# Kernel tuning notes

Hardware: AMD Instinct MI355X
Metric: run time of the kernel (lower is better)

Reference implementation:

```python
import jax, jax.numpy as jnp
from jax import lax
import numpy as np

B, N, K = 8, 4096, 64          # clouds, points per cloud, max neighbors
N1, N2 = N // 2, N // 8        # fps ratio 0.5, then 0.25
R1, R2 = 0.2, 0.4              # ball-query radii


def setup_inputs() -> dict:
    key = jax.random.key(0)
    ks = jax.random.split(key, 7)
    def w(k, i, o):
        return jax.random.normal(k, (i, o), jnp.float32) / np.sqrt(i).astype(np.float32)
    return {
        "pos": jax.random.uniform(ks[0], (B, N, 3), jnp.float32),
        "w1a": w(ks[1], 3, 64),    "b1a": jnp.zeros(64, jnp.float32),
        "w1b": w(ks[2], 64, 64),   "b1b": jnp.zeros(64, jnp.float32),
        "w2a": w(ks[3], 67, 128),  "b2a": jnp.zeros(128, jnp.float32),
        "w2b": w(ks[4], 128, 128), "b2b": jnp.zeros(128, jnp.float32),
        "w3a": w(ks[5], 131, 256), "b3a": jnp.zeros(256, jnp.float32),
        "w3b": w(ks[6], 256, 1024),"b3b": jnp.zeros(1024, jnp.float32),
    }


def fps(pos, n_samples):
    # farthest point sampling, deterministic start at index 0. pos: [n, 3]
    d0 = jnp.sum((pos - pos[0]) ** 2, axis=-1)
    def step(mind, _):
        nxt = jnp.argmax(mind)
        d = jnp.sum((pos - pos[nxt]) ** 2, axis=-1)
        return jnp.minimum(mind, d), nxt
    _, idxs = lax.scan(step, d0, None, length=n_samples - 1)
    return jnp.concatenate([jnp.zeros((1,), idxs.dtype), idxs])


def ball_query(centers, pts, r):
    # up to K neighbors within radius r (nearest-first); centers are a subset of pts
    d2 = jnp.sum((centers[:, None, :] - pts[None, :, :]) ** 2, axis=-1)  # [M, n]
    neg = jnp.where(d2 <= r * r, -d2, -jnp.inf)
    vals, nbr = lax.top_k(neg, K)
    return nbr, vals > -jnp.inf  # [M, K] indices, validity mask


def mlp(x, w1, b1, w2, b2, relu_last):
    h = jax.nn.relu(x @ w1 + b1) @ w2 + b2
    return jax.nn.relu(h) if relu_last else h


def masked_max(h, mask):
    # max over neighbor axis; every center has itself as a valid neighbor
    return jnp.max(jnp.where(mask[..., None], h, -jnp.inf), axis=1)


def reference(pos, w1a, b1a, w1b, b1b, w2a, b2a, w2b, b2b, w3a, b3a, w3b, b3b):
    def single(p):  # p: [N, 3]
        # SA1: x is None -> per-edge input is relative position only
        idx1 = fps(p, N1)
        c1 = p[idx1]                                   # [N1, 3]
        nbr1, m1 = ball_query(c1, p, R1)               # [N1, K]
        rel1 = p[nbr1] - c1[:, None, :]                # [N1, K, 3]
        x1 = masked_max(mlp(rel1, w1a, b1a, w1b, b1b, True), m1)   # [N1, 64]
        # SA2: per-edge input is [x_j, pos_j - pos_i]
        idx2 = fps(c1, N2)
        c2 = c1[idx2]                                  # [N2, 3]
        nbr2, m2 = ball_query(c2, c1, R2)              # [N2, K]
        feat2 = jnp.concatenate([x1[nbr2], c1[nbr2] - c2[:, None, :]], axis=-1)  # [N2,K,67]
        x2 = masked_max(mlp(feat2, w2a, b2a, w2b, b2b, True), m2)  # [N2, 128]
        # Global SA: MLP on [x, pos] then global max pool
        g = mlp(jnp.concatenate([x2, c2], axis=-1), w3a, b3a, w3b, b3b, False)   # [N2,1024]
        return jnp.max(g, axis=0)                      # [1024]
    return jax.vmap(single)(pos)                       # [B, 1024]
```

## Files before the change

kernel.cpp:

```cpp
#include <hip/hip_runtime.h>
#include <cstdint>
#include <cstddef>


static constexpr int Bc = 8;
static constexpr int Np = 4096;
static constexpr int Kn = 64;
static constexpr int M1 = 2048;
static constexpr int M2 = 512;
static constexpr int LDX = 132;

#define DEVINL __device__ __forceinline__

DEVINL float d2_exact(float ax, float ay, float az, float bx, float by, float bz) {
    float dx = __fsub_rn(ax, bx);
    float dy = __fsub_rn(ay, by);
    float dz = __fsub_rn(az, bz);
    float xx = __fmul_rn(dx, dx);
    float yy = __fmul_rn(dy, dy);
    float zz = __fmul_rn(dz, dz);
    return __fadd_rn(__fadd_rn(xx, yy), zz);
}

template <int CTRL, int RM, int BM>
DEVINL unsigned long long dpp_max_step(unsigned long long k) {
    unsigned lo = (unsigned)k, hi = (unsigned)(k >> 32);
    unsigned slo = (unsigned)__builtin_amdgcn_update_dpp(0, (int)lo, CTRL, RM, BM, true);
    unsigned shi = (unsigned)__builtin_amdgcn_update_dpp(0, (int)hi, CTRL, RM, BM, true);
    unsigned long long s = ((unsigned long long)shi << 32) | (unsigned long long)slo;
    return s > k ? s : k;
}

DEVINL unsigned long long wave_max_u64_dpp(unsigned long long k) {
    k = dpp_max_step<0x111, 0xf, 0xf>(k);
    k = dpp_max_step<0x112, 0xf, 0xf>(k);
    k = dpp_max_step<0x114, 0xf, 0xf>(k);
    k = dpp_max_step<0x118, 0xf, 0xf>(k);
    k = dpp_max_step<0x142, 0xa, 0xf>(k);
    k = dpp_max_step<0x143, 0xc, 0xf>(k);
    return k;
}

DEVINL unsigned mort3(unsigned v) {
    return (v & 1u) | ((v & 2u) << 2) | ((v & 4u) << 4);
}

DEVINL unsigned cell_of(float x, float y, float z) {
    int ix = (int)(x * 8.0f); ix = ix < 0 ? 0 : (ix > 7 ? 7 : ix);
    int iy = (int)(y * 8.0f); iy = iy < 0 ? 0 : (iy > 7 ? 7 : iy);
    int iz = (int)(z * 8.0f); iz = iz < 0 ? 0 : (iz > 7 ? 7 : iz);
    return mort3((unsigned)ix) | (mort3((unsigned)iy) << 1) | (mort3((unsigned)iz) << 2);
}

DEVINL unsigned* scan512(unsigned* h0, unsigned* h1, int t) {
    unsigned* src = h0; unsigned* dst = h1;
    for (int d = 1; d < 512; d <<= 1) {
        unsigned v = src[t];
        if (t >= d) v += src[t - d];
        dst[t] = v;
        __syncthreads();
        unsigned* tmp = src; src = dst; dst = tmp;
    }
    return src;
}

__global__ __launch_bounds__(512)
void fps2x_kernel(const float* __restrict__ pos, float* __restrict__ c1,
                  float* __restrict__ c2, float* __restrict__ X) {
    constexpr int NT = 512;
    __shared__ float scx[Np], scy[Np], scz[Np];
    __shared__ unsigned spk[Np];
    __shared__ float s2c[M1 * 3];
    __shared__ unsigned h0[512], h1[512];
    __shared__ unsigned long long slots[3];
    const int b = blockIdx.x;
    const int t = threadIdx.x;
    const int lane = t & 63;

    {
        constexpr int PT = Np / NT;
        const float* base = pos + (size_t)b * Np * 3;
        float gx[PT], gy[PT], gz[PT];
        unsigned gc[PT];
        #pragma unroll
        for (int j = 0; j < PT; ++j) {
            int p = j * NT + t;
            gx[j] = base[p * 3 + 0];
            gy[j] = base[p * 3 + 1];
            gz[j] = base[p * 3 + 2];
            gc[j] = cell_of(gx[j], gy[j], gz[j]);
        }
        float x0 = base[0], y0 = base[1], z0 = base[2];
        h0[t] = 0;
        if (t == 0) { slots[0] = 0; slots[1] = 0; slots[2] = 0; }
        __syncthreads();
        #pragma unroll
        for (int j = 0; j < PT; ++j) atomicAdd(&h0[gc[j]], 1u);
        __syncthreads();
        unsigned cnt = h0[t];
        unsigned* inc = scan512(h0, h1, t);
        inc[t] -= cnt;
        __syncthreads();
        #pragma unroll
        for (int j = 0; j < PT; ++j) {
            unsigned p = atomicAdd(&inc[gc[j]], 1u);
            scx[p] = gx[j]; scy[p] = gy[j]; scz[p] = gz[j];
            spk[p] = ((0xFFFu - (unsigned)(j * NT + t)) << 12) | p;
        }
        __syncthreads();

        float px[PT], py[PT], pz[PT], mind[PT];
        unsigned oi[PT];
        #pragma unroll
        for (int j = 0; j < PT; ++j) {
            int p = t * PT + j;
            px[j] = scx[p]; py[j] = scy[p]; pz[j] = scz[p];
            oi[j] = spk[p];
        }
        float lox = px[0], hix = px[0], loy = py[0], hiy = py[0], loz = pz[0], hiz = pz[0];
        #pragma unroll
        for (int j = 1; j < PT; ++j) {
            lox = fminf(lox, px[j]); hix = fmaxf(hix, px[j]);
            loy = fminf(loy, py[j]); hiy = fmaxf(hiy, py[j]);
            loz = fminf(loz, pz[j]); hiz = fmaxf(hiz, pz[j]);
        }

        unsigned long long ck = 0;
        #pragma unroll
        for (int j = 0; j < PT; ++j) {
            float d = d2_exact(px[j], py[j], pz[j], x0, y0, z0);
            mind[j] = d;
            unsigned long long kj =
                ((unsigned long long)__float_as_uint(d) << 24) | (unsigned long long)oi[j];
            if (kj > ck) ck = kj;
        }
        float bmax = __uint_as_float((unsigned)(ck >> 24));
        unsigned long long wkey = wave_max_u64_dpp(ck);
        if (lane == 63) atomicMax(&slots[1], wkey);
        if (t == 0) {
            s2c[0] = x0; s2c[1] = y0; s2c[2] = z0;
        }
        int rd = 1, wr = 2, rs = 0;
        for (int s = 1; s < M1; ++s) {
            __syncthreads();
            unsigned long long km = slots[rd];
            if (t == 0) slots[rs] = 0;
            unsigned spos = (unsigned)km & 0xFFFu;
            float cx = scx[spos], cy = scy[spos], cz = scz[spos];
            if (t == 0) {
                s2c[s * 3 + 0] = cx; s2c[s * 3 + 1] = cy; s2c[s * 3 + 2] = cz;
            }
            float dxv = fmaxf(fmaxf(lox - cx, cx - hix), 0.0f);
            float dyv = fmaxf(fmaxf(loy - cy, cy - hiy), 0.0f);
            float dzv = fmaxf(fmaxf(loz - cz, cz - hiz), 0.0f);
            float L = dxv * dxv + dyv * dyv + dzv * dzv;
            bool fire = (L * 0.999f <= bmax);
            if (fire) {
                unsigned long long nck = 0;
                #pragma unroll
                for (int j = 0; j < PT; ++j) {
                    float d = d2_exact(px[j], py[j], pz[j], cx, cy, cz);
                    float m = fminf(mind[j], d);
                    mind[j] = m;
                    unsigned long long kj =
                        ((unsigned long long)__float_as_uint(m) << 24) | (unsigned long long)oi[j];
                    if (kj > nck) nck = kj;
                }
                ck = nck;
                bmax = __uint_as_float((unsigned)(ck >> 24));
            }
            if (__ballot(fire) != 0ull) wkey = wave_max_u64_dpp(ck);
            if (lane == 63) atomicMax(&slots[wr], wkey);
            int nrd = wr; wr = rs; rs = rd; rd = nrd;
        }
    }
    __syncthreads();

    for (int i = t; i < M1 * 3; i += 512)
        c1[(size_t)b * M1 * 3 + i] = s2c[i];

    {
        constexpr int PT = M1 / NT;
        float* c2buf = s2c;
        float gx[PT], gy[PT], gz[PT];
        unsigned gc[PT];
        #pragma unroll
        for (int j = 0; j < PT; ++j) {
            int p = j * NT + t;
            gx[j] = s2c[p * 3 + 0];
            gy[j] = s2c[p * 3 + 1];
            gz[j] = s2c[p * 3 + 2];
            gc[j] = cell_of(gx[j], gy[j], gz[j]);
        }
        float x0 = s2c[0], y0 = s2c[1], z0 = s2c[2];
        h0[t] = 0;
        if (t == 0) { slots[0] = 0; slots[1] = 0; slots[2] = 0; }
        __syncthreads();
        #pragma unroll
        for (int j = 0; j < PT; ++j) atomicAdd(&h0[gc[j]], 1u);
        __syncthreads();
        unsigned cnt = h0[t];
        unsigned* inc = scan512(h0, h1, t);
        inc[t] -= cnt;
        __syncthreads();
        #pragma unroll
        for (int j = 0; j < PT; ++j) {
            unsigned p = atomicAdd(&inc[gc[j]], 1u);
            scx[p] = gx[j]; scy[p] = gy[j]; scz[p] = gz[j];
            spk[p] = ((0xFFFu - (unsigned)(j * NT + t)) << 12) | p;
        }
        __syncthreads();

        float px[PT], py[PT], pz[PT], mind[PT];
        unsigned oi[PT];
        #pragma unroll
        for (int j = 0; j < PT; ++j) {
            int p = t * PT + j;
            px[j] = scx[p]; py[j] = scy[p]; pz[j] = scz[p];
            oi[j] = spk[p];
        }
        float lox = px[0], hix = px[0], loy = py[0], hiy = py[0], loz = pz[0], hiz = pz[0];
        #pragma unroll
        for (int j = 1; j < PT; ++j) {
            lox = fminf(lox, px[j]); hix = fmaxf(hix, px[j]);
            loy = fminf(loy, py[j]); hiy = fmaxf(hiy, py[j]);
            loz = fminf(loz, pz[j]); hiz = fmaxf(hiz, pz[j]);
        }

        unsigned long long ck = 0;
        #pragma unroll
        for (int j = 0; j < PT; ++j) {
            float d = d2_exact(px[j], py[j], pz[j], x0, y0, z0);
            mind[j] = d;
            unsigned long long kj =
                ((unsigned long long)__float_as_uint(d) << 24) | (unsigned long long)oi[j];
            if (kj > ck) ck = kj;
        }
        float bmax = __uint_as_float((unsigned)(ck >> 24));
        unsigned long long wkey = wave_max_u64_dpp(ck);
        if (lane == 63) atomicMax(&slots[1], wkey);
        if (t == 0) {
            c2buf[0] = x0; c2buf[1] = y0; c2buf[2] = z0;
        }
        int rd = 1, wr = 2, rs = 0;
        for (int s = 1; s < M2; ++s) {
            __syncthreads();
            unsigned long long km = slots[rd];
            if (t == 0) slots[rs] = 0;
            unsigned spos = (unsigned)km & 0xFFFu;
            float cx = scx[spos], cy = scy[spos], cz = scz[spos];
            if (t == 0) {
                c2buf[s * 3 + 0] = cx; c2buf[s * 3 + 1] = cy; c2buf[s * 3 + 2] = cz;
            }
            float dxv = fmaxf(fmaxf(lox - cx, cx - hix), 0.0f);
            float dyv = fmaxf(fmaxf(loy - cy, cy - hiy), 0.0f);
            float dzv = fmaxf(fmaxf(loz - cz, cz - hiz), 0.0f);
            float L = dxv * dxv + dyv * dyv + dzv * dzv;
            bool fire = (L * 0.999f <= bmax);
            if (fire) {
                unsigned long long nck = 0;
                #pragma unroll
                for (int j = 0; j < PT; ++j) {
                    float d = d2_exact(px[j], py[j], pz[j], cx, cy, cz);
                    float m = fminf(mind[j], d);
                    mind[j] = m;
                    unsigned long long kj =
                        ((unsigned long long)__float_as_uint(m) << 24) | (unsigned long long)oi[j];
                    if (kj > nck) nck = kj;
                }
                ck = nck;
                bmax = __uint_as_float((unsigned)(ck >> 24));
            }
            if (__ballot(fire) != 0ull) wkey = wave_max_u64_dpp(ck);
            if (lane == 63) atomicMax(&slots[wr], wkey);
            int nrd = wr; wr = rs; rs = rd; rd = nrd;
        }
        __syncthreads();

        for (int i = t; i < M2 * 3; i += 512)
            c2[(size_t)b * M2 * 3 + i] = c2buf[i];
        for (int i = t; i < M2 * 3; i += 512) {
            int s = i / 3, k = i - s * 3;
            X[(size_t)(b * M2 + s) * LDX + 128 + k] = c2buf[i];
        }
    }
}

template <int NPT>
__global__ __launch_bounds__(256)
void bq_kernel(const float* __restrict__ pts, const float* __restrict__ ctr,
               int mshift, float r2, int* __restrict__ nbr) {
    constexpr int CH = NPT / 64;
    constexpr int CAP = 1024;
    __shared__ uint2 cbuf[4][CAP];
    const int lane = threadIdx.x & 63;
    const int wl = threadIdx.x >> 6;
    int w = __builtin_amdgcn_readfirstlane((int)(blockIdx.x * 4 + wl));
    const int b = w >> mshift;
    const float* pb = pts + (size_t)b * NPT * 3;
    const float* cp = ctr + (size_t)w * 3;
    float cx = cp[0], cy = cp[1], cz = cp[2];
    const unsigned r2b = __float_as_uint(r2);

    unsigned ub[CH];
    int cnt = 0;
    #pragma unroll
    for (int j = 0; j < CH; ++j) {
        int p = j * 64 + lane;
        float d = d2_exact(pb[p * 3 + 0], pb[p * 3 + 1], pb[p * 3 + 2], cx, cy, cz);
        ub[j] = __float_as_uint(d);
        cnt += __popcll(__ballot(ub[j] <= r2b));
    }
    int* out = nbr + (size_t)w * Kn;
    const unsigned long long lml = (1ull << lane) - 1ull;

    if (cnt <= Kn) {
        int basep = 0;
        #pragma unroll
        for (int j = 0; j < CH; ++j) {
            bool v = ub[j] <= r2b;
            unsigned long long mk = __ballot(v);
            if (v) out[basep + __popcll(mk & lml)] = j * 64 + lane;
            basep += __popcll(mk);
        }
        if (lane >= cnt) out[lane] = -1;
    } else if (cnt <= CAP) {
        uint2* buf = cbuf[wl];
        int basep = 0;
        #pragma unroll
        for (int j = 0; j < CH; ++j) {
            bool v = ub[j] <= r2b;
            unsigned long long mk = __ballot(v);
            if (v) buf[basep + __popcll(mk & lml)] =
                       make_uint2(ub[j], (unsigned)(j * 64 + lane));
            basep += __popcll(mk);
        }
        const int C2 = (cnt + 63) >> 6;
        unsigned cb[CAP / 64], ci[CAP / 64];
        #pragma unroll
        for (int e = 0; e < CAP / 64; ++e) {
            if (e >= C2) break;
            int p = e * 64 + lane;
            uint2 v = buf[p];
            cb[e] = (p < cnt) ? v.x : 0xFFFFFFFFu;
            ci[e] = v.y;
        }
        unsigned lo = 0, hi = r2b;
        while (lo < hi) {
            unsigned mid = lo + ((hi - lo) >> 1);
            int c = 0;
            #pragma unroll
            for (int e = 0; e < CAP / 64; ++e) {
                if (e >= C2) break;
                c += __popcll(__ballot(cb[e] <= mid));
            }
            if (c >= Kn) hi = mid; else lo = mid + 1;
        }
        const unsigned tt = lo;
        int cntLess = 0;
        #pragma unroll
        for (int e = 0; e < CAP / 64; ++e) {
            if (e >= C2) break;
            cntLess += __popcll(__ballot(cb[e] < tt));
        }
        const int quota = Kn - cntLess;
        int baseLt = 0, eqseen = 0;
        #pragma unroll
        for (int e = 0; e < CAP / 64; ++e) {
            if (e >= C2) break;
            bool lt = cb[e] < tt;
            bool eq = cb[e] == tt;
            unsigned long long mlt = __ballot(lt);
            unsigned long long meq = __ballot(eq);
            if (lt) out[baseLt + __popcll(mlt & lml)] = (int)ci[e];
            if (eq) {
                int rr = eqseen + __popcll(meq & lml);
                if (rr < quota) out[cntLess + rr] = (int)ci[e];
            }
            baseLt += __popcll(mlt);
            eqseen += __popcll(meq);
        }
    } else {
        unsigned lo = 0, hi = r2b;
        while (lo < hi) {
            unsigned mid = lo + ((hi - lo) >> 1);
            int c = 0;
            #pragma unroll
            for (int j = 0; j < CH; ++j) c += __popcll(__ballot(ub[j] <= mid));
            if (c >= Kn) hi = mid; else lo = mid + 1;
        }
        const unsigned tt = lo;
        int cntLess = 0;
        #pragma unroll
        for (int j = 0; j < CH; ++j) cntLess += __popcll(__ballot(ub[j] < tt));
        const int quota = Kn - cntLess;
        int baseLt = 0, eqseen = 0;
        #pragma unroll
        for (int j = 0; j < CH; ++j) {
            bool lt = ub[j] < tt;
            bool eq = ub[j] == tt;
            unsigned long long mlt = __ballot(lt);
            unsigned long long meq = __ballot(eq);
            if (lt) out[baseLt + __popcll(mlt & lml)] = j * 64 + lane;
            if (eq) {
                int rr = eqseen + __popcll(meq & lml);
                if (rr < quota) out[cntLess + rr] = j * 64 + lane;
            }
            baseLt += __popcll(mlt);
            eqseen += __popcll(meq);
        }
    }
}

__global__ __launch_bounds__(256)
void mlp1_kernel(const float* __restrict__ pos, const float* __restrict__ c1,
                 const int* __restrict__ nbr, const float* __restrict__ w1aT,
                 const float* __restrict__ w1bT, const float* __restrict__ b1b,
                 float* __restrict__ x1) {
    const int lane = threadIdx.x & 63;
    int w = __builtin_amdgcn_readfirstlane((int)(blockIdx.x * 4 + (threadIdx.x >> 6)));
    const int b = w >> 11;
    const int ii = nbr[(size_t)w * Kn + lane];
    const bool valid = ii >= 0;
    const int i2 = valid ? ii : 0;
    const float* pp = pos + ((size_t)b * Np + i2) * 3;
    const float* cc = c1 + (size_t)w * 3;
    float rx = pp[0] - cc[0], ry = pp[1] - cc[1], rz = pp[2] - cc[2];
    float h1[64];
    #pragma unroll
    for (int h = 0; h < 64; ++h) {
        float4 wv = ((const float4*)w1aT)[h];
        float a = fmaf(rx, wv.x, fmaf(ry, wv.y, fmaf(rz, wv.z, wv.w)));
        h1[h] = fmaxf(a, 0.0f);
    }
    float* orow = x1 + (size_t)w * 64;
    for (int c4 = 0; c4 < 16; ++c4) {
        float v4[4];
        #pragma unroll
        for (int cq = 0; cq < 4; ++cq) {
            int c = c4 * 4 + cq;
            float acc = b1b[c];
            const float4* wr = (const float4*)(w1bT + (size_t)c * 64);
            #pragma unroll
            for (int q = 0; q < 16; ++q) {
                float4 wv = wr[q];
                acc = fmaf(h1[4 * q + 0], wv.x, acc);
                acc = fmaf(h1[4 * q + 1], wv.y, acc);
                acc = fmaf(h1[4 * q + 2], wv.z, acc);
                acc = fmaf(h1[4 * q + 3], wv.w, acc);
            }
            float v = fmaxf(acc, 0.0f);
            v = valid ? v : -__builtin_inff();
            #pragma unroll
            for (int o = 32; o > 0; o >>= 1) v = fmaxf(v, __shfl_xor(v, o, 64));
            v4[cq] = v;
        }
        if (lane == 0)
            ((float4*)orow)[c4] = make_float4(v4[0], v4[1], v4[2], v4[3]);
    }
}

__global__ __launch_bounds__(256)
void mlp2_kernel(const float* __restrict__ x1, const float* __restrict__ c1,
                 const float* __restrict__ c2, const int* __restrict__ nbr2,
                 const float* __restrict__ w2aT, const float* __restrict__ w2bT,
                 const float* __restrict__ b2b, float* __restrict__ X) {
    const int lane = threadIdx.x & 63;
    int w = __builtin_amdgcn_readfirstlane((int)(blockIdx.x * 4 + (threadIdx.x >> 6)));
    const int b = w >> 9;
    const int ii = nbr2[(size_t)w * Kn + lane];
    const bool valid = ii >= 0;
    const int i2 = valid ? ii : 0;

    float x[68];
    const float4* xr = (const float4*)(x1 + ((size_t)b * M1 + i2) * 64);
// ... 85 lines not shown
    const int col0 = nt * 64;
    const int t = threadIdx.x;
    const int rg = t >> 5, cg = t & 31;

    float acc[4][2] = {{0.f, 0.f}, {0.f, 0.f}, {0.f, 0.f}, {0.f, 0.f}};
    for (int k0 = 0; k0 < 256; k0 += 32) {
        #pragma unroll
        for (int q = 0; q < 4; ++q) {
            int id = t + q * 256;
            As[id >> 5][id & 31] = H[(size_t)(row0 + (id >> 5)) * 256 + k0 + (id & 31)];
        }
        #pragma unroll
        for (int q = 0; q < 8; ++q) {
            int id = t + q * 256;
            Bs[id >> 6][id & 63] = w3b[(size_t)(k0 + (id >> 6)) * 1024 + col0 + (id & 63)];
        }
        __syncthreads();
        #pragma unroll
        for (int kk = 0; kk < 32; ++kk) {
            float b0 = Bs[kk][cg * 2 + 0];
            float b1 = Bs[kk][cg * 2 + 1];
            #pragma unroll
            for (int j = 0; j < 4; ++j) {
                float a = As[rg * 4 + j][kk];
                acc[j][0] = fmaf(a, b0, acc[j][0]);
                acc[j][1] = fmaf(a, b1, acc[j][1]);
            }
        }
        __syncthreads();
    }
    float m0 = fmaxf(fmaxf(acc[0][0], acc[1][0]), fmaxf(acc[2][0], acc[3][0]));
    float m1 = fmaxf(fmaxf(acc[0][1], acc[1][1]), fmaxf(acc[2][1], acc[3][1]));
    red[rg][cg * 2 + 0] = m0;
    red[rg][cg * 2 + 1] = m1;
    __syncthreads();
    if (t < 64) {
        float v = red[0][t];
        #pragma unroll
        for (int q = 1; q < 8; ++q) v = fmaxf(v, red[q][t]);
        part[((size_t)b * 16 + mt) * 1024 + col0 + t] = v;
    }
}

__global__ __launch_bounds__(256)
void rmax_kernel(const float* __restrict__ part, const float* __restrict__ b3b,
                 float* __restrict__ out) {
    int i = blockIdx.x * 256 + threadIdx.x;
    int b = i >> 10, c = i & 1023;
    float v = -__builtin_inff();
    #pragma unroll
    for (int tt = 0; tt < 16; ++tt)
        v = fmaxf(v, part[((size_t)b * 16 + tt) * 1024 + c]);
    out[i] = v + b3b[c];
}

__global__ __launch_bounds__(256)
void prep_kernel(const float* __restrict__ w1a, const float* __restrict__ b1a,
                 const float* __restrict__ w1b, const float* __restrict__ w2a,
                 const float* __restrict__ b2a, const float* __restrict__ w2b,
                 float* __restrict__ w1aT, float* __restrict__ w1bT,
                 float* __restrict__ w2aT, float* __restrict__ w2bT) {
    int i = blockIdx.x * 256 + threadIdx.x;
    if (i < 64 * 4) {
        int h = i >> 2, d = i & 3;
        w1aT[i] = (d < 3) ? w1a[d * 64 + h] : b1a[h];
    }
    if (i < 64 * 64) {
        int c = i >> 6, h = i & 63;
        w1bT[i] = w1b[h * 64 + c];
    }
    if (i < 128 * 80) {
        int h = i / 80, d = i - h * 80;
        w2aT[i] = (d < 67) ? w2a[d * 128 + h] : ((d == 67) ? b2a[h] : 0.0f);
    }
    {
        int c = i >> 7, h = i & 127;
        w2bT[i] = w2b[h * 128 + c];
    }
}

extern "C" void kernel_launch(void* const* d_in, const int* in_sizes, int n_in,
                              void* d_out, int out_size, void* d_ws, size_t ws_size,
                              hipStream_t stream) {
    const float* pos = (const float*)d_in[0];
    const float* w1a = (const float*)d_in[1];
    const float* b1a = (const float*)d_in[2];
    const float* w1b = (const float*)d_in[3];
    const float* b1b = (const float*)d_in[4];
    const float* w2a = (const float*)d_in[5];
    const float* b2a = (const float*)d_in[6];
    const float* w2b = (const float*)d_in[7];
    const float* b2b = (const float*)d_in[8];
    const float* w3a = (const float*)d_in[9];
    const float* b3a = (const float*)d_in[10];
    const float* w3b = (const float*)d_in[11];
    const float* b3b = (const float*)d_in[12];
    float* out = (float*)d_out;

    char* ws = (char*)d_ws;
    size_t off = 0;
    auto alloc = [&](size_t bytes) -> char* {
        char* p = ws + off;
        off += (bytes + 255) & ~(size_t)255;
        return p;
    };
    float* c1   = (float*)alloc(sizeof(float) * Bc * M1 * 3);
    float* c2   = (float*)alloc(sizeof(float) * Bc * M2 * 3);
    int*   nbr1 = (int*)alloc(sizeof(int) * Bc * M1 * Kn);
    int*   nbr2 = (int*)alloc(sizeof(int) * Bc * M2 * Kn);
    float* x1   = (float*)alloc(sizeof(float) * Bc * M1 * 64);
    float* X    = (float*)alloc(sizeof(float) * Bc * M2 * LDX);
    float* H    = (float*)alloc(sizeof(float) * Bc * M2 * 256);
    float* part = (float*)alloc(sizeof(float) * Bc * 16 * 1024);
    float* w1aT = (float*)alloc(sizeof(float) * 64 * 4);
    float* w1bT = (float*)alloc(sizeof(float) * 64 * 64);
    float* w2aT = (float*)alloc(sizeof(float) * 128 * 80);
    float* w2bT = (float*)alloc(sizeof(float) * 128 * 128);

    prep_kernel<<<dim3(64), dim3(256), 0, stream>>>(w1a, b1a, w1b, w2a, b2a, w2b,
                                                    w1aT, w1bT, w2aT, w2bT);
    fps2x_kernel<<<dim3(Bc), dim3(512), 0, stream>>>(pos, c1, c2, X);
    bq_kernel<Np><<<dim3(Bc * M1 / 4), dim3(256), 0, stream>>>(
        pos, c1, 11, (float)(0.2 * 0.2), nbr1);
    mlp1_kernel<<<dim3(Bc * M1 / 4), dim3(256), 0, stream>>>(
        pos, c1, nbr1, w1aT, w1bT, b1b, x1);
    bq_kernel<M1><<<dim3(Bc * M2 / 4), dim3(256), 0, stream>>>(
        c1, c2, 9, (float)(0.4 * 0.4), nbr2);
    mlp2_kernel<<<dim3(Bc * M2 / 4), dim3(256), 0, stream>>>(
        x1, c1, c2, nbr2, w2aT, w2bT, b2b, X);
    gemm1_kernel<<<dim3(Bc * M2), dim3(256), 0, stream>>>(X, w3a, b3a, H);
    gemm2_kernel<<<dim3(Bc * 16 * 16), dim3(256), 0, stream>>>(H, w3b, part);
    rmax_kernel<<<dim3(32), dim3(256), 0, stream>>>(part, b3b, out);
}
```

Before: 2.569 ms.

## Replace FPS shared atomicMax argmax with per-wave slots and 32-bit DPP reduction

In both farthest-point-sampling loops, the 64-bit packed key reduction is split into a 32-bit DPP max on the distance bits plus a tie-break on the index, using readlane and ballot. The shared-memory atomicMax into a triple-buffered slot is replaced by each wave writing its candidate to a double-buffered per-wave array, which every thread then reduces over 8 entries after the barrier. This removes the 64-bit DPP pairs, the LDS atomics and the slot-reset bookkeeping from the serial per-sample critical path. In exchange each thread does extra vector LDS loads and compares per step, and the tie-break path adds a second reduction when distances collide.

After: 2.741 ms. 6.7% more time.

```diff
diff --git a/kernel.cpp b/kernel.cpp
--- a/kernel.cpp
+++ b/kernel.cpp
@@ -23,22 +23,33 @@
 }
 
 template <int CTRL, int RM, int BM>
-DEVINL unsigned long long dpp_max_step(unsigned long long k) {
-    unsigned lo = (unsigned)k, hi = (unsigned)(k >> 32);
-    unsigned slo = (unsigned)__builtin_amdgcn_update_dpp(0, (int)lo, CTRL, RM, BM, true);
-    unsigned shi = (unsigned)__builtin_amdgcn_update_dpp(0, (int)hi, CTRL, RM, BM, true);
-    unsigned long long s = ((unsigned long long)shi << 32) | (unsigned long long)slo;
-    return s > k ? s : k;
-}
-
-DEVINL unsigned long long wave_max_u64_dpp(unsigned long long k) {
-    k = dpp_max_step<0x111, 0xf, 0xf>(k);
-    k = dpp_max_step<0x112, 0xf, 0xf>(k);
-    k = dpp_max_step<0x114, 0xf, 0xf>(k);
-    k = dpp_max_step<0x118, 0xf, 0xf>(k);
-    k = dpp_max_step<0x142, 0xa, 0xf>(k);
-    k = dpp_max_step<0x143, 0xc, 0xf>(k);
-    return k;
+DEVINL unsigned dpp_max_u32_step(unsigned v) {
+    unsigned s = (unsigned)__builtin_amdgcn_update_dpp(0, (int)v, CTRL, RM, BM, true);
+    return s > v ? s : v;
+}
+
+DEVINL unsigned wave_max_u32_dpp(unsigned v) {
+    v = dpp_max_u32_step<0x111, 0xf, 0xf>(v);
+    v = dpp_max_u32_step<0x112, 0xf, 0xf>(v);
+    v = dpp_max_u32_step<0x114, 0xf, 0xf>(v);
+    v = dpp_max_u32_step<0x118, 0xf, 0xf>(v);
+    v = dpp_max_u32_step<0x142, 0xa, 0xf>(v);
+    v = dpp_max_u32_step<0x143, 0xc, 0xf>(v);
+    return v;
+}
+
+DEVINL void wave_reduce_cand(unsigned ch, unsigned cl, unsigned& wh, unsigned& wl) {
+    unsigned h = wave_max_u32_dpp(ch);
+    wh = (unsigned)__builtin_amdgcn_readlane((int)h, 63);
+    unsigned long long mask = __ballot(ch == wh);
+    if (__popcll(mask) == 1) {
+        int ln = __ffsll((unsigned long long)mask) - 1;
+        wl = (unsigned)__builtin_amdgcn_readlane((int)cl, ln);
+    } else {
+        unsigned lm = (ch == wh) ? cl : 0u;
+        lm = wave_max_u32_dpp(lm);
+        wl = (unsigned)__builtin_amdgcn_readlane((int)lm, 63);
+    }
 }
 
 DEVINL unsigned mort3(unsigned v) {
@@ -72,10 +83,11 @@
     __shared__ unsigned spk[Np];
     __shared__ float s2c[M1 * 3];
     __shared__ unsigned h0[512], h1[512];
-    __shared__ unsigned long long slots[3];
+    __shared__ __align__(16) unsigned long long wslot[2][8];
     const int b = blockIdx.x;
     const int t = threadIdx.x;
     const int lane = t & 63;
+    const int wid = t >> 6;
 
     {
         constexpr int PT = Np / NT;
@@ -92,7 +104,6 @@
         }
         float x0 = base[0], y0 = base[1], z0 = base[2];
         h0[t] = 0;
-        if (t == 0) { slots[0] = 0; slots[1] = 0; slots[2] = 0; }
         __syncthreads();
         #pragma unroll
         for (int j = 0; j < PT; ++j) atomicAdd(&h0[gc[j]], 1u);
@@ -125,27 +136,39 @@
             loz = fminf(loz, pz[j]); hiz = fmaxf(hiz, pz[j]);
         }
 
-        unsigned long long ck = 0;
+        unsigned ch = 0, cl = 0;
         #pragma unroll
         for (int j = 0; j < PT; ++j) {
             float d = d2_exact(px[j], py[j], pz[j], x0, y0, z0);
             mind[j] = d;
-            unsigned long long kj =
-                ((unsigned long long)__float_as_uint(d) << 24) | (unsigned long long)oi[j];
-            if (kj > ck) ck = kj;
-        }
-        float bmax = __uint_as_float((unsigned)(ck >> 24));
-        unsigned long long wkey = wave_max_u64_dpp(ck);
-        if (lane == 63) atomicMax(&slots[1], wkey);
+            unsigned db = __float_as_uint(d);
+            ch = db > ch ? db : ch;
+        }
+        #pragma unroll
+        for (int j = 0; j < PT; ++j)
+            if (__float_as_uint(mind[j]) == ch && oi[j] > cl) cl = oi[j];
+        float bmax = __uint_as_float(ch);
+
+        unsigned cwh, cwl;
+        wave_reduce_cand(ch, cl, cwh, cwl);
+        if (lane == 0)
+            wslot[1][wid] = (((unsigned long long)cwh) << 32) | cwl;
         if (t == 0) {
             s2c[0] = x0; s2c[1] = y0; s2c[2] = z0;
         }
-        int rd = 1, wr = 2, rs = 0;
         for (int s = 1; s < M1; ++s) {
             __syncthreads();
-            unsigned long long km = slots[rd];
-            if (t == 0) slots[rs] = 0;
-            unsigned spos = (unsigned)km & 0xFFFu;
+            int rb = s & 1;
+            const ulonglong2* sp = (const ulonglong2*)&wslot[rb][0];
+            ulonglong2 q0 = sp[0], q1 = sp[1], q2 = sp[2], q3 = sp[3];
+            unsigned long long m0 = q0.x > q0.y ? q0.x : q0.y;
+            unsigned long long m1 = q1.x > q1.y ? q1.x : q1.y;
+            unsigned long long m2 = q2.x > q2.y ? q2.x : q2.y;
+            unsigned long long m3 = q3.x > q3.y ? q3.x : q3.y;
+            m0 = m0 > m1 ? m0 : m1;
+            m2 = m2 > m3 ? m2 : m3;
+            unsigned long long wk = m0 > m2 ? m0 : m2;
+            unsigned spos = (unsigned)wk & 0xFFFu;
             float cx = scx[spos], cy = scy[spos], cz = scz[spos];
             if (t == 0) {
                 s2c[s * 3 + 0] = cx; s2c[s * 3 + 1] = cy; s2c[s * 3 + 2] = cz;
@@ -156,22 +179,25 @@
             float L = dxv * dxv + dyv * dyv + dzv * dzv;
             bool fire = (L * 0.999f <= bmax);
             if (fire) {
-                unsigned long long nck = 0;
+                unsigned nh = 0;
                 #pragma unroll
                 for (int j = 0; j < PT; ++j) {
                     float d = d2_exact(px[j], py[j], pz[j], cx, cy, cz);
                     float m = fminf(mind[j], d);
                     mind[j] = m;
-                    unsigned long long kj =
-                        ((unsigned long long)__float_as_uint(m) << 24) | (unsigned long long)oi[j];
-                    if (kj > nck) nck = kj;
+                    unsigned mb = __float_as_uint(m);
+                    nh = mb > nh ? mb : nh;
                 }
-                ck = nck;
-                bmax = __uint_as_float((unsigned)(ck >> 24));
-            }
-            if (__ballot(fire) != 0ull) wkey = wave_max_u64_dpp(ck);
-            if (lane == 63) atomicMax(&slots[wr], wkey);
-            int nrd = wr; wr = rs; rs = rd; rd = nrd;
+                unsigned nl = 0;
+                #pragma unroll
+                for (int j = 0; j < PT; ++j)
+                    if (__float_as_uint(mind[j]) == nh && oi[j] > nl) nl = oi[j];
+                ch = nh; cl = nl;
+                bmax = __uint_as_float(ch);
+            }
+            if (__ballot(fire) != 0ull) wave_reduce_cand(ch, cl, cwh, cwl);
+            if (lane == 0)
+                wslot[rb ^ 1][wid] = (((unsigned long long)cwh) << 32) | cwl;
         }
     }
     __syncthreads();
@@ -194,7 +220,6 @@
         }
         float x0 = s2c[0], y0 = s2c[1], z0 = s2c[2];
         h0[t] = 0;
-        if (t == 0) { slots[0] = 0; slots[1] = 0; slots[2] = 0; }
         __syncthreads();
         #pragma unroll
         for (int j = 0; j < PT; ++j) atomicAdd(&h0[gc[j]], 1u);
@@ -227,27 +252,39 @@
             loz = fminf(loz, pz[j]); hiz = fmaxf(hiz, pz[j]);
         }
 
-        unsigned long long ck = 0;
+        unsigned ch = 0, cl = 0;
         #pragma unroll
         for (int j = 0; j < PT; ++j) {
             float d = d2_exact(px[j], py[j], pz[j], x0, y0, z0);
             mind[j] = d;
-            unsigned long long kj =
-                ((unsigned long long)__float_as_uint(d) << 24) | (unsigned long long)oi[j];
-            if (kj > ck) ck = kj;
-        }
-        float bmax = __uint_as_float((unsigned)(ck >> 24));
-        unsigned long long wkey = wave_max_u64_dpp(ck);
-        if (lane == 63) atomicMax(&slots[1], wkey);
+            unsigned db = __float_as_uint(d);
+            ch = db > ch ? db : ch;
+        }
+        #pragma unroll
+        for (int j = 0; j < PT; ++j)
+            if (__float_as_uint(mind[j]) == ch && oi[j] > cl) cl = oi[j];
+        float bmax = __uint_as_float(ch);
+
+        unsigned cwh, cwl;
+        wave_reduce_cand(ch, cl, cwh, cwl);
+        if (lane == 0)
+            wslot[1][wid] = (((unsigned long long)cwh) << 32) | cwl;
         if (t == 0) {
             c2buf[0] = x0; c2buf[1] = y0; c2buf[2] = z0;
         }
-        int rd = 1, wr = 2, rs = 0;
         for (int s = 1; s < M2; ++s) {
             __syncthreads();
-            unsigned long long km = slots[rd];
-            if (t == 0) slots[rs] = 0;
-            unsigned spos = (unsigned)km & 0xFFFu;
+            int rb = s & 1;
+            const ulonglong2* sp = (const ulonglong2*)&wslot[rb][0];
+            ulonglong2 q0 = sp[0], q1 = sp[1], q2 = sp[2], q3 = sp[3];
+            unsigned long long m0 = q0.x > q0.y ? q0.x : q0.y;
+            unsigned long long m1 = q1.x > q1.y ? q1.x : q1.y;
+            unsigned long long m2 = q2.x > q2.y ? q2.x : q2.y;
+            unsigned long long m3 = q3.x > q3.y ? q3.x : q3.y;
+            m0 = m0 > m1 ? m0 : m1;
+            m2 = m2 > m3 ? m2 : m3;
+            unsigned long long wk = m0 > m2 ? m0 : m2;
+            unsigned spos = (unsigned)wk & 0xFFFu;
             float cx = scx[spos], cy = scy[spos], cz = scz[spos];
             if (t == 0) {
                 c2buf[s * 3 + 0] = cx; c2buf[s * 3 + 1] = cy; c2buf[s * 3 + 2] = cz;
@@ -258,22 +295,25 @@
             float L = dxv * dxv + dyv * dyv + dzv * dzv;
             bool fire = (L * 0.999f <= bmax);
             if (fire) {
-                unsigned long long nck = 0;
+                unsigned nh = 0;
                 #pragma unroll
                 for (int j = 0; j < PT; ++j) {
                     float d = d2_exact(px[j], py[j], pz[j], cx, cy, cz);
                     float m = fminf(mind[j], d);
                     mind[j] = m;
-                    unsigned long long kj =
-                        ((unsigned long long)__float_as_uint(m) << 24) | (unsigned long long)oi[j];
-                    if (kj > nck) nck = kj;
+                    unsigned mb = __float_as_uint(m);
+                    nh = mb > nh ? mb : nh;
                 }
-                ck = nck;
-                bmax = __uint_as_float((unsigned)(ck >> 24));
-            }
-            if (__ballot(fire) != 0ull) wkey = wave_max_u64_dpp(ck);
-            if (lane == 63) atomicMax(&slots[wr], wkey);
-            int nrd = wr; wr = rs; rs = rd; rd = nrd;
+                unsigned nl = 0;
+                #pragma unroll
+                for (int j = 0; j < PT; ++j)
+                    if (__float_as_uint(mind[j]) == nh && oi[j] > nl) nl = oi[j];
+                ch = nh; cl = nl;
+                bmax = __uint_as_float(ch);
+            }
+            if (__ballot(fire) != 0ull) wave_reduce_cand(ch, cl, cwh, cwl);
+            if (lane == 0)
+                wslot[rb ^ 1][wid] = (((unsigned long long)cwh) << 32) | cwl;
         }
         __syncthreads();
 
```

## Split FPS stages and co-schedule them with independent ball-query and MLP work

Applied to the files above, without the earlier changes.

The two-stage FPS kernel is split. Stage one is merged with the weight-prep kernel as extra blocks. Stage two runs in its own 256-thread block alongside the SA1 ball-query blocks in the same launch, since both depend only on c1. The SA2 ball query is likewise fused with the SA1 MLP, so the long serial FPS2 loop on 8 blocks overlaps with the independent parallel work and the launch count drops. Point storage moves to a packed float4 LDS layout for single-load center fetches. In exchange, the 256-thread FPS2 has more points per thread, and the fused kernels carry the larger LDS of their biggest role.

New measurement: 2.393 ms. -6.8%, faster.

```diff
diff --git a/kernel.cpp b/kernel.cpp
--- a/kernel.cpp
+++ b/kernel.cpp
@@ -64,238 +64,165 @@
     return src;
 }
 
+DEVINL unsigned* scan512x256(unsigned* h0, unsigned* h1, int t) {
+    unsigned* src = h0; unsigned* dst = h1;
+    for (int d = 1; d < 512; d <<= 1) {
+        unsigned a = src[t];
+        unsigned b = src[t + 256];
+        if (t >= d) a += src[t - d];
+        b += src[t + 256 - d];
+        dst[t] = a; dst[t + 256] = b;
+        __syncthreads();
+        unsigned* tmp = src; src = dst; dst = tmp;
+    }
+    return src;
+}
+
 __global__ __launch_bounds__(512)
-void fps2x_kernel(const float* __restrict__ pos, float* __restrict__ c1,
-                  float* __restrict__ c2, float* __restrict__ X) {
-    constexpr int NT = 512;
-    __shared__ float scx[Np], scy[Np], scz[Np];
-    __shared__ unsigned spk[Np];
+void fps1_prep_kernel(const float* __restrict__ pos, float* __restrict__ c1,
+                      const float* __restrict__ w1a, const float* __restrict__ b1a,
+                      const float* __restrict__ w1b, const float* __restrict__ w2a,
+                      const float* __restrict__ b2a, const float* __restrict__ w2b,
+                      float* __restrict__ w1aT, float* __restrict__ w1bT,
+                      float* __restrict__ w2aT, float* __restrict__ w2bT) {
+    __shared__ float4 scp[Np];
     __shared__ float s2c[M1 * 3];
     __shared__ unsigned h0[512], h1[512];
     __shared__ unsigned long long slots[3];
+    const int t = threadIdx.x;
+
+    if (blockIdx.x >= Bc) {
+        int i = (int)(blockIdx.x - Bc) * 512 + t;
+        if (i < 64 * 4) {
+            int h = i >> 2, d = i & 3;
+            w1aT[i] = (d < 3) ? w1a[d * 64 + h] : b1a[h];
+        }
+        if (i < 64 * 64) {
+            int c = i >> 6, h = i & 63;
+            w1bT[i] = w1b[h * 64 + c];
+        }
+        if (i < 128 * 80) {
+            int h = i / 80, d = i - h * 80;
+            w2aT[i] = (d < 67) ? w2a[d * 128 + h] : ((d == 67) ? b2a[h] : 0.0f);
+        }
+        {
+            int c = i >> 7, h = i & 127;
+            w2bT[i] = w2b[h * 128 + c];
+        }
+        return;
+    }
+
     const int b = blockIdx.x;
-    const int t = threadIdx.x;
     const int lane = t & 63;
-
-    {
-        constexpr int PT = Np / NT;
-        const float* base = pos + (size_t)b * Np * 3;
-        float gx[PT], gy[PT], gz[PT];
-        unsigned gc[PT];
-        #pragma unroll
-        for (int j = 0; j < PT; ++j) {
-            int p = j * NT + t;
-            gx[j] = base[p * 3 + 0];
-            gy[j] = base[p * 3 + 1];
-            gz[j] = base[p * 3 + 2];
-            gc[j] = cell_of(gx[j], gy[j], gz[j]);
-        }
-        float x0 = base[0], y0 = base[1], z0 = base[2];
-        h0[t] = 0;
-        if (t == 0) { slots[0] = 0; slots[1] = 0; slots[2] = 0; }
+    constexpr int NT = 512;
+    constexpr int PT = Np / NT;
+
+    const float* base = pos + (size_t)b * Np * 3;
+    float gx[PT], gy[PT], gz[PT];
+    unsigned gc[PT];
+    #pragma unroll
+    for (int j = 0; j < PT; ++j) {
+        int p = j * NT + t;
+        gx[j] = base[p * 3 + 0];
+        gy[j] = base[p * 3 + 1];
+        gz[j] = base[p * 3 + 2];
+        gc[j] = cell_of(gx[j], gy[j], gz[j]);
+    }
+    float x0 = base[0], y0 = base[1], z0 = base[2];
+    h0[t] = 0;
+    if (t == 0) { slots[0] = 0; slots[1] = 0; slots[2] = 0; }
+    __syncthreads();
+    #pragma unroll
+    for (int j = 0; j < PT; ++j) atomicAdd(&h0[gc[j]], 1u);
+    __syncthreads();
+    unsigned cnt = h0[t];
+    unsigned* inc = scan512(h0, h1, t);
+    inc[t] -= cnt;
+    __syncthreads();
+    #pragma unroll
+    for (int j = 0; j < PT; ++j) {
+        unsigned p = atomicAdd(&inc[gc[j]], 1u);
+        unsigned key = ((0xFFFu - (unsigned)(j * NT + t)) << 12) | p;
+        scp[p] = make_float4(gx[j], gy[j], gz[j], __uint_as_float(key));
+    }
+    __syncthreads();
+
+    float px[PT], py[PT], pz[PT], mind[PT];
+    unsigned oi[PT];
+    #pragma unroll
+    for (int j = 0; j < PT; ++j) {
+        float4 v = scp[t * PT + j];
+        px[j] = v.x; py[j] = v.y; pz[j] = v.z;
+        oi[j] = __float_as_uint(v.w);
+    }
+    float lox = px[0], hix = px[0], loy = py[0], hiy = py[0], loz = pz[0], hiz = pz[0];
+    #pragma unroll
+    for (int j = 1; j < PT; ++j) {
+        lox = fminf(lox, px[j]); hix = fmaxf(hix, px[j]);
+        loy = fminf(loy, py[j]); hiy = fmaxf(hiy, py[j]);
+        loz = fminf(loz, pz[j]); hiz = fmaxf(hiz, pz[j]);
+    }
+
+    unsigned long long ck = 0;
+    #pragma unroll
+    for (int j = 0; j < PT; ++j) {
+        float d = d2_exact(px[j], py[j], pz[j], x0, y0, z0);
+        mind[j] = d;
+        unsigned long long kj =
+            ((unsigned long long)__float_as_uint(d) << 24) | (unsigned long long)oi[j];
+        if (kj > ck) ck = kj;
+    }
+    float bmax = __uint_as_float((unsigned)(ck >> 24));
+    unsigned long long wkey = wave_max_u64_dpp(ck);
+    if (lane == 63) atomicMax(&slots[1], wkey);
+    if (t == 0) {
+        s2c[0] = x0; s2c[1] = y0; s2c[2] = z0;
+    }
+    int rd = 1, wr = 2, rs = 0;
+    for (int s = 1; s < M1; ++s) {
         __syncthreads();
-        #pragma unroll
-        for (int j = 0; j < PT; ++j) atomicAdd(&h0[gc[j]], 1u);
-        __syncthreads();
-        unsigned cnt = h0[t];
-        unsigned* inc = scan512(h0, h1, t);
-        inc[t] -= cnt;
-        __syncthreads();
-        #pragma unroll
-        for (int j = 0; j < PT; ++j) {
-            unsigned p = atomicAdd(&inc[gc[j]], 1u);
-            scx[p] = gx[j]; scy[p] = gy[j]; scz[p] = gz[j];
-            spk[p] = ((0xFFFu - (unsigned)(j * NT + t)) << 12) | p;
-        }
-        __syncthreads();
-
-        float px[PT], py[PT], pz[PT], mind[PT];
-        unsigned oi[PT];
-        #pragma unroll
-        for (int j = 0; j < PT; ++j) {
-            int p = t * PT + j;
-            px[j] = scx[p]; py[j] = scy[p]; pz[j] = scz[p];
-            oi[j] = spk[p];
-        }
-        float lox = px[0], hix = px[0], loy = py[0], hiy = py[0], loz = pz[0], hiz = pz[0];
-        #pragma unroll
-        for (int j = 1; j < PT; ++j) {
-            lox = fminf(lox, px[j]); hix = fmaxf(hix, px[j]);
-            loy = fminf(loy, py[j]); hiy = fmaxf(hiy, py[j]);
-            loz = fminf(loz, pz[j]); hiz = fmaxf(hiz, pz[j]);
-        }
-
-        unsigned long long ck = 0;
-        #pragma unroll
-        for (int j = 0; j < PT; ++j) {
-            float d = d2_exact(px[j], py[j], pz[j], x0, y0, z0);
-            mind[j] = d;
-            unsigned long long kj =
-                ((unsigned long long)__float_as_uint(d) << 24) | (unsigned long long)oi[j];
-            if (kj > ck) ck = kj;
-        }
-        float bmax = __uint_as_float((unsigned)(ck >> 24));
-        unsigned long long wkey = wave_max_u64_dpp(ck);
-        if (lane == 63) atomicMax(&slots[1], wkey);
+        unsigned long long km = slots[rd];
+        if (t == 0) slots[rs] = 0;
+        unsigned spos = (unsigned)km & 0xFFFu;
+        float4 cc = scp[spos];
+        float cx = cc.x, cy = cc.y, cz = cc.z;
         if (t == 0) {
-            s2c[0] = x0; s2c[1] = y0; s2c[2] = z0;
-        }
-        int rd = 1, wr = 2, rs = 0;
-        for (int s = 1; s < M1; ++s) {
-            __syncthreads();
-            unsigned long long km = slots[rd];
-            if (t == 0) slots[rs] = 0;
-            unsigned spos = (unsigned)km & 0xFFFu;
-            float cx = scx[spos], cy = scy[spos], cz = scz[spos];
-            if (t == 0) {
-                s2c[s * 3 + 0] = cx; s2c[s * 3 + 1] = cy; s2c[s * 3 + 2] = cz;
+            s2c[s * 3 + 0] = cx; s2c[s * 3 + 1] = cy; s2c[s * 3 + 2] = cz;
+        }
+        float dxv = fmaxf(fmaxf(lox - cx, cx - hix), 0.0f);
+        float dyv = fmaxf(fmaxf(loy - cy, cy - hiy), 0.0f);
+        float dzv = fmaxf(fmaxf(loz - cz, cz - hiz), 0.0f);
+        float L = dxv * dxv + dyv * dyv + dzv * dzv;
+        bool fire = (L * 0.999f <= bmax);
+        if (fire) {
+            unsigned long long nck = 0;
+            #pragma unroll
+            for (int j = 0; j < PT; ++j) {
+                float d = d2_exact(px[j], py[j], pz[j], cx, cy, cz);
+                float m = fminf(mind[j], d);
+                mind[j] = m;
+                unsigned long long kj =
+                    ((unsigned long long)__float_as_uint(m) << 24) | (unsigned long long)oi[j];
+                if (kj > nck) nck = kj;
             }
-            float dxv = fmaxf(fmaxf(lox - cx, cx - hix), 0.0f);
-            float dyv = fmaxf(fmaxf(loy - cy, cy - hiy), 0.0f);
-            float dzv = fmaxf(fmaxf(loz - cz, cz - hiz), 0.0f);
-            float L = dxv * dxv + dyv * dyv + dzv * dzv;
-            bool fire = (L * 0.999f <= bmax);
-            if (fire) {
-                unsigned long long nck = 0;
-                #pragma unroll
-                for (int j = 0; j < PT; ++j) {
-                    float d = d2_exact(px[j], py[j], pz[j], cx, cy, cz);
-                    float m = fminf(mind[j], d);
-                    mind[j] = m;
-                    unsigned long long kj =
-                        ((unsigned long long)__float_as_uint(m) << 24) | (unsigned long long)oi[j];
-                    if (kj > nck) nck = kj;
-                }
-                ck = nck;
-                bmax = __uint_as_float((unsigned)(ck >> 24));
-            }
-            if (__ballot(fire) != 0ull) wkey = wave_max_u64_dpp(ck);
-            if (lane == 63) atomicMax(&slots[wr], wkey);
-            int nrd = wr; wr = rs; rs = rd; rd = nrd;
-        }
-    }
-    __syncthreads();
-
+            ck = nck;
+            bmax = __uint_as_float((unsigned)(ck >> 24));
+        }
+        if (__ballot(fire) != 0ull) wkey = wave_max_u64_dpp(ck);
+        if (lane == 63) atomicMax(&slots[wr], wkey);
+        int nrd = wr; wr = rs; rs = rd; rd = nrd;
+    }
+    __syncthreads();
     for (int i = t; i < M1 * 3; i += 512)
         c1[(size_t)b * M1 * 3 + i] = s2c[i];
-
-    {
-        constexpr int PT = M1 / NT;
-        float* c2buf = s2c;
-        float gx[PT], gy[PT], gz[PT];
-        unsigned gc[PT];
-        #pragma unroll
-        for (int j = 0; j < PT; ++j) {
-            int p = j * NT + t;
-            gx[j] = s2c[p * 3 + 0];
-            gy[j] = s2c[p * 3 + 1];
-            gz[j] = s2c[p * 3 + 2];
-            gc[j] = cell_of(gx[j], gy[j], gz[j]);
-        }
-        float x0 = s2c[0], y0 = s2c[1], z0 = s2c[2];
-        h0[t] = 0;
-        if (t == 0) { slots[0] = 0; slots[1] = 0; slots[2] = 0; }
-        __syncthreads();
-        #pragma unroll
-        for (int j = 0; j < PT; ++j) atomicAdd(&h0[gc[j]], 1u);
-        __syncthreads();
-        unsigned cnt = h0[t];
-        unsigned* inc = scan512(h0, h1, t);
-        inc[t] -= cnt;
-        __syncthreads();
-        #pragma unroll
-        for (int j = 0; j < PT; ++j) {
-            unsigned p = atomicAdd(&inc[gc[j]], 1u);
-            scx[p] = gx[j]; scy[p] = gy[j]; scz[p] = gz[j];
-            spk[p] = ((0xFFFu - (unsigned)(j * NT + t)) << 12) | p;
-        }
-        __syncthreads();
-
-        float px[PT], py[PT], pz[PT], mind[PT];
-        unsigned oi[PT];
-        #pragma unroll
-        for (int j = 0; j < PT; ++j) {
-            int p = t * PT + j;
-            px[j] = scx[p]; py[j] = scy[p]; pz[j] = scz[p];
-            oi[j] = spk[p];
-        }
-        float lox = px[0], hix = px[0], loy = py[0], hiy = py[0], loz = pz[0], hiz = pz[0];
-        #pragma unroll
-        for (int j = 1; j < PT; ++j) {
-            lox = fminf(lox, px[j]); hix = fmaxf(hix, px[j]);
-            loy = fminf(loy, py[j]); hiy = fmaxf(hiy, py[j]);
-            loz = fminf(loz, pz[j]); hiz = fmaxf(hiz, pz[j]);
-        }
-
-        unsigned long long ck = 0;
-        #pragma unroll
-        for (int j = 0; j < PT; ++j) {
-            float d = d2_exact(px[j], py[j], pz[j], x0, y0, z0);
-            mind[j] = d;
-            unsigned long long kj =
-                ((unsigned long long)__float_as_uint(d) << 24) | (unsigned long long)oi[j];
-            if (kj > ck) ck = kj;
-        }
-        float bmax = __uint_as_float((unsigned)(ck >> 24));
-        unsigned long long wkey = wave_max_u64_dpp(ck);
-        if (lane == 63) atomicMax(&slots[1], wkey);
-        if (t == 0) {
-            c2buf[0] = x0; c2buf[1] = y0; c2buf[2] = z0;
-        }
-        int rd = 1, wr = 2, rs = 0;
-        for (int s = 1; s < M2; ++s) {
-            __syncthreads();
-            unsigned long long km = slots[rd];
-            if (t == 0) slots[rs] = 0;
-            unsigned spos = (unsigned)km & 0xFFFu;
-            float cx = scx[spos], cy = scy[spos], cz = scz[spos];
-            if (t == 0) {
-                c2buf[s * 3 + 0] = cx; c2buf[s * 3 + 1] = cy; c2buf[s * 3 + 2] = cz;
-            }
-            float dxv = fmaxf(fmaxf(lox - cx, cx - hix), 0.0f);
-            float dyv = fmaxf(fmaxf(loy - cy, cy - hiy), 0.0f);
-            float dzv = fmaxf(fmaxf(loz - cz, cz - hiz), 0.0f);
-            float L = dxv * dxv + dyv * dyv + dzv * dzv;
-            bool fire = (L * 0.999f <= bmax);
-            if (fire) {
-                unsigned long long nck = 0;
-                #pragma unroll
-                for (int j = 0; j < PT; ++j) {
-                    float d = d2_exact(px[j], py[j], pz[j], cx, cy, cz);
-                    float m = fminf(mind[j], d);
-                    mind[j] = m;
-                    unsigned long long kj =
-                        ((unsigned long long)__float_as_uint(m) << 24) | (unsigned long long)oi[j];
-                    if (kj > nck) nck = kj;
-                }
-                ck = nck;
-                bmax = __uint_as_float((unsigned)(ck >> 24));
-            }
-            if (__ballot(fire) != 0ull) wkey = wave_max_u64_dpp(ck);
-            if (lane == 63) atomicMax(&slots[wr], wkey);
-            int nrd = wr; wr = rs; rs = rd; rd = nrd;
-        }
-        __syncthreads();
-
-        for (int i = t; i < M2 * 3; i += 512)
-            c2[(size_t)b * M2 * 3 + i] = c2buf[i];
-        for (int i = t; i < M2 * 3; i += 512) {
-            int s = i / 3, k = i - s * 3;
-            X[(size_t)(b * M2 + s) * LDX + 128 + k] = c2buf[i];
-        }
-    }
 }
 
 template <int NPT>
-__global__ __launch_bounds__(256)
-void bq_kernel(const float* __restrict__ pts, const float* __restrict__ ctr,
-               int mshift, float r2, int* __restrict__ nbr) {
+DEVINL void bq_body(const float* __restrict__ pts, const float* __restrict__ ctr,
+                    int mshift, float r2, int* __restrict__ nbr,
+                    uint2* __restrict__ buf, int w, int lane) {
     constexpr int CH = NPT / 64;
     constexpr int CAP = 1024;
-    __shared__ uint2 cbuf[4][CAP];
-    const int lane = threadIdx.x & 63;
-    const int wl = threadIdx.x >> 6;
-    int w = __builtin_amdgcn_readfirstlane((int)(blockIdx.x * 4 + wl));
     const int b = w >> mshift;
     const float* pb = pts + (size_t)b * NPT * 3;
     const float* cp = ctr + (size_t)w * 3;
@@ -325,7 +252,6 @@
         }
         if (lane >= cnt) out[lane] = -1;
     } else if (cnt <= CAP) {
-        uint2* buf = cbuf[wl];
         int basep = 0;
         #pragma unroll
         for (int j = 0; j < CH; ++j) {
@@ -412,15 +338,159 @@
     }
 }
 
+static constexpr int K2_LDS = 43040;
+
 __global__ __launch_bounds__(256)
-void mlp1_kernel(const float* __restrict__ pos, const float* __restrict__ c1,
-                 const int* __restrict__ nbr, const float* __restrict__ w1aT,
-                 const float* __restrict__ w1bT, const float* __restrict__ b1b,
-                 float* __restrict__ x1) {
-    const int lane = threadIdx.x & 63;
-    int w = __builtin_amdgcn_readfirstlane((int)(blockIdx.x * 4 + (threadIdx.x >> 6)));
+void fps2_bq1_kernel(const float* __restrict__ pos, const float* __restrict__ c1,
+                     float* __restrict__ c2, float* __restrict__ X,
+                     int* __restrict__ nbr1) {
+    extern __shared__ char smem[];
+    const int t = threadIdx.x;
+    const int lane = t & 63;
+
+    if (blockIdx.x >= Bc) {
+        uint2* buf = (uint2*)smem + (size_t)(t >> 6) * 1024;
+        int w = __builtin_amdgcn_readfirstlane(
+            (int)(blockIdx.x - Bc) * 4 + (t >> 6));
+        bq_body<Np>(pos, c1, 11, (float)(0.2 * 0.2), nbr1, buf, w, lane);
+        return;
+    }
+
+    float4* scp2 = (float4*)smem;
+    float* c2buf = (float*)(smem + 32768);
+    unsigned* h0 = (unsigned*)(smem + 38912);
+    unsigned* h1 = (unsigned*)(smem + 40960);
+    unsigned long long* slots = (unsigned long long*)(smem + 43008);
+
+    const int b = blockIdx.x;
+    constexpr int NT = 256;
+    constexpr int PT = M1 / NT;
+    const float* base = c1 + (size_t)b * M1 * 3;
+
+    float gx[PT], gy[PT], gz[PT];
+    unsigned gc[PT];
+    #pragma unroll
+    for (int j = 0; j < PT; ++j) {
+        int p = j * NT + t;
+        gx[j] = base[p * 3 + 0];
+        gy[j] = base[p * 3 + 1];
+        gz[j] = base[p * 3 + 2];
+        gc[j] = cell_of(gx[j], gy[j], gz[j]);
+    }
+    float x0 = base[0], y0 = base[1], z0 = base[2];
+    h0[t] = 0; h0[t + 256] = 0;
+    if (t == 0) { slots[0] = 0; slots[1] = 0; slots[2] = 0; }
+    __syncthreads();
+    #pragma unroll
+    for (int j = 0; j < PT; ++j) atomicAdd(&h0[gc[j]], 1u);
+    __syncthreads();
+    unsigned cnt0 = h0[t], cnt1 = h0[t + 256];
+    unsigned* inc = scan512x256(h0, h1, t);
+    inc[t] -= cnt0; inc[t + 256] -= cnt1;
+    __syncthreads();
+    #pragma unroll
+    for (int j = 0; j < PT; ++j) {
+        unsigned p = atomicAdd(&inc[gc[j]], 1u);
+        unsigned key = ((0xFFFu - (unsigned)(j * NT + t)) << 12) | p;
+        scp2[p] = make_float4(gx[j], gy[j], gz[j], __uint_as_float(key));
+    }
+    __syncthreads();
+
+    float px[PT], py[PT], pz[PT], mind[PT];
+    unsigned oi[PT];
+    #pragma unroll
+    for (int j = 0; j < PT; ++j) {
+        float4 v = scp2[t * PT + j];
+        px[j] = v.x; py[j] = v.y; pz[j] = v.z;
+        oi[j] = __float_as_uint(v.w);
+    }
+    float lox = px[0], hix = px[0], loy = py[0], hiy = py[0], loz = pz[0], hiz = pz[0];
+    #pragma unroll
+    for (int j = 1; j < PT; ++j) {
+        lox = fminf(lox, px[j]); hix = fmaxf(hix, px[j]);
+        loy = fminf(loy, py[j]); hiy = fmaxf(hiy, py[j]);
+        loz = fminf(loz, pz[j]); hiz = fmaxf(hiz, pz[j]);
+    }
+
+    unsigned long long ck = 0;
+    #pragma unroll
+    for (int j = 0; j < PT; ++j) {
+        float d = d2_exact(px[j], py[j], pz[j], x0, y0, z0);
+        mind[j] = d;
+        unsigned long long kj =
+            ((unsigned long long)__float_as_uint(d) << 24) | (unsigned long long)oi[j];
+        if (kj > ck) ck = kj;
+    }
+    float bmax = __uint_as_float((unsigned)(ck >> 24));
+    unsigned long long wkey = wave_max_u64_dpp(ck);
+    if (lane == 63) atomicMax(&slots[1], wkey);
+    if (t == 0) {
+        c2buf[0] = x0; c2buf[1] = y0; c2buf[2] = z0;
+    }
+    int rd = 1, wr = 2, rs = 0;
+    for (int s = 1; s < M2; ++s) {
+        __syncthreads();
+        unsigned long long km = slots[rd];
+        if (t == 0) slots[rs] = 0;
+        unsigned spos = (unsigned)km & 0xFFFu;
+        float4 cc = scp2[spos];
+        float cx = cc.x, cy = cc.y, cz = cc.z;
+        if (t == 0) {
+            c2buf[s * 3 + 0] = cx; c2buf[s * 3 + 1] = cy; c2buf[s * 3 + 2] = cz;
+        }
+        float dxv = fmaxf(fmaxf(lox - cx, cx - hix), 0.0f);
+        float dyv = fmaxf(fmaxf(loy - cy, cy - hiy), 0.0f);
+        float dzv = fmaxf(fmaxf(loz - cz, cz - hiz), 0.0f);
+        float L = dxv * dxv + dyv * dyv + dzv * dzv;
+        bool fire = (L * 0.999f <= bmax);
+        if (fire) {
+            unsigned long long nck = 0;
+            #pragma unroll
+            for (int j = 0; j < PT; ++j) {
+                float d = d2_exact(px[j], py[j], pz[j], cx, cy, cz);
+                float m = fminf(mind[j], d);
+                mind[j] = m;
+                unsigned long long kj =
+                    ((unsigned long long)__float_as_uint(m) << 24) | (unsigned long long)oi[j];
+                if (kj > nck) nck = kj;
+            }
+            ck = nck;
+            bmax = __uint_as_float((unsigned)(ck >> 24));
+        }
+        if (__ballot(fire) != 0ull) wkey = wave_max_u64_dpp(ck);
+        if (lane == 63) atomicMax(&slots[wr], wkey);
+        int nrd = wr; wr = rs; rs = rd; rd = nrd;
+    }
+    __syncthreads();
+    for (int i = t; i < M2 * 3; i += 256)
+        c2[(size_t)b * M2 * 3 + i] = c2buf[i];
+    for (int i = t; i < M2 * 3; i += 256) {
+        int s = i / 3, k = i - s * 3;
+        X[(size_t)(b * M2 + s) * LDX + 128 + k] = c2buf[i];
+    }
+}
+
+__global__ __launch_bounds__(256)
+void bq2_mlp1_kernel(const float* __restrict__ pos, const float* __restrict__ c1,
+                     const float* __restrict__ c2, int* __restrict__ nbr2,
+                     const int* __restrict__ nbr1, const float* __restrict__ w1aT,
+                     const float* __restrict__ w1bT, const float* __restrict__ b1b,
+                     float* __restrict__ x1) {
+    __shared__ uint2 cbuf[4][1024];
+    const int t = threadIdx.x;
+    const int lane = t & 63;
+    constexpr int NBQ2 = Bc * M2 / 4;
+
+    if (blockIdx.x < NBQ2) {
+        int w = __builtin_amdgcn_readfirstlane((int)blockIdx.x * 4 + (t >> 6));
+        bq_body<M1>(c1, c2, 9, (float)(0.4 * 0.4), nbr2, cbuf[t >> 6], w, lane);
+        return;
+    }
+
+    int w = __builtin_amdgcn_readfirstlane(
+        (int)(blockIdx.x - NBQ2) * 4 + (t >> 6));
     const int b = w >> 11;
-    const int ii = nbr[(size_t)w * Kn + lane];
+    const int ii = nbr1[(size_t)w * Kn + lane];
     const bool valid = ii >= 0;
     const int i2 = valid ? ii : 0;
     const float* pp = pos + ((size_t)b * Np + i2) * 3;
@@ -612,31 +682,6 @@
     for (int tt = 0; tt < 16; ++tt)
         v = fmaxf(v, part[((size_t)b * 16 + tt) * 1024 + c]);
     out[i] = v + b3b[c];
-}
-
-__global__ __launch_bounds__(256)
-void prep_kernel(const float* __restrict__ w1a, const float* __restrict__ b1a,
-                 const float* __restrict__ w1b, const float* __restrict__ w2a,
-                 const float* __restrict__ b2a, const float* __restrict__ w2b,
-                 float* __restrict__ w1aT, float* __restrict__ w1bT,
-                 float* __restrict__ w2aT, float* __restrict__ w2bT) {
-    int i = blockIdx.x * 256 + threadIdx.x;
-    if (i < 64 * 4) {
-        int h = i >> 2, d = i & 3;
-        w1aT[i] = (d < 3) ? w1a[d * 64 + h] : b1a[h];
-    }
-    if (i < 64 * 64) {
-        int c = i >> 6, h = i & 63;
-        w1bT[i] = w1b[h * 64 + c];
-    }
-    if (i < 128 * 80) {
-        int h = i / 80, d = i - h * 80;
-        w2aT[i] = (d < 67) ? w2a[d * 128 + h] : ((d == 67) ? b2a[h] : 0.0f);
-    }
-    {
-        int c = i >> 7, h = i & 127;
-        w2bT[i] = w2b[h * 128 + c];
-    }
 }
 
 extern "C" void kernel_launch(void* const* d_in, const int* in_sizes, int n_in,
@@ -677,15 +722,12 @@
     float* w2aT = (float*)alloc(sizeof(float) * 128 * 80);
     float* w2bT = (float*)alloc(sizeof(float) * 128 * 128);
 
-    prep_kernel<<<dim3(64), dim3(256), 0, stream>>>(w1a, b1a, w1b, w2a, b2a, w2b,
-                                                    w1aT, w1bT, w2aT, w2bT);
-    fps2x_kernel<<<dim3(Bc), dim3(512), 0, stream>>>(pos, c1, c2, X);
-    bq_kernel<Np><<<dim3(Bc * M1 / 4), dim3(256), 0, stream>>>(
-        pos, c1, 11, (float)(0.2 * 0.2), nbr1);
-    mlp1_kernel<<<dim3(Bc * M1 / 4), dim3(256), 0, stream>>>(
-        pos, c1, nbr1, w1aT, w1bT, b1b, x1);
-    bq_kernel<M1><<<dim3(Bc * M2 / 4), dim3(256), 0, stream>>>(
-        c1, c2, 9, (float)(0.4 * 0.4), nbr2);
+    fps1_prep_kernel<<<dim3(Bc + 32), dim3(512), 0, stream>>>(
+        pos, c1, w1a, b1a, w1b, w2a, b2a, w2b, w1aT, w1bT, w2aT, w2bT);
+    fps2_bq1_kernel<<<dim3(Bc + Bc * M1 / 4), dim3(256), K2_LDS, stream>>>(
+        pos, c1, c2, X, nbr1);
+    bq2_mlp1_kernel<<<dim3(Bc * M2 / 4 + Bc * M1 / 4), dim3(256), 0, stream>>>(
+        pos, c1, c2, nbr2, nbr1, w1aT, w1bT, b1b, x1);
     mlp2_kernel<<<dim3(Bc * M2 / 4), dim3(256), 0, stream>>>(
         x1, c1, c2, nbr2, w2aT, w2bT, b2b, X);
     gemm1_kernel<<<dim3(Bc * M2), dim3(256), 0, stream>>>(X, w3a, b3a, H);
```
